# Performance work log

Measured on AMD Instinct MI355X. Metric: run time of the kernel, lower is better.

Reference implementation:

```python
import jax, jax.numpy as jnp
import numpy as np

U = 50  # lstm units

def lstm_seq(x, Wx, Wh, b):
    # x: [B,S,D] -> h: [B,S,U], Keras LSTMCell gate order i,f,g,o
    B = x.shape[0]
    xz = jnp.einsum('bsd,dk->bsk', x, Wx) + b  # [B,S,4U]
    def step(carry, zt):
        h, c = carry
        z = zt + h @ Wh
        i, f, g, o = jnp.split(z, 4, axis=-1)
        c = jax.nn.sigmoid(f) * c + jax.nn.sigmoid(i) * jnp.tanh(g)
        h = jax.nn.sigmoid(o) * jnp.tanh(c)
        return (h, c), h
    init = (jnp.zeros((B, U), x.dtype), jnp.zeros((B, U), x.dtype))
    _, hs = jax.lax.scan(step, init, jnp.swapaxes(xz, 0, 1))
    return jnp.swapaxes(hs, 0, 1)

def bilstm(x, fWx, fWh, fb, bWx, bWh, bb):
    # Keras RNN(go_backwards=True) does NOT re-reverse outputs; concat as-is.
    fw = lstm_seq(x, fWx, fWh, fb)
    bw = lstm_seq(x[:, ::-1, :], bWx, bWh, bb)
    return jnp.concatenate([fw, bw], axis=-1)

def local_inference(x1e, m1, x2e, m2):
    # Literal translation: inputs are batch-first [B,S,D]; the TF code transposes
    # to [S,B,D] and batch-matmuls over the leading (seq) axis, so attention is
    # over the batch index at each timestep. A[s,i,j] = x1e[i,s]. x2e[j,s]
    A = jnp.einsum('isd,jsd->sij', x1e, x2e)
    m1t = m1.T  # [S,B]
    m2t = m2.T
    w2 = jnp.exp(A - jnp.max(A, axis=2, keepdims=True)) * m2t[:, None, :]
    alpha = w2 / (jnp.sum(w2, axis=-1, keepdims=True) + 1e-8)
    x1_dual = jnp.einsum('sij,jsd->isd', alpha, x2e)  # [B,S,D]
    A1 = A - jnp.max(A, axis=1, keepdims=True)
    w1 = jnp.exp(jnp.swapaxes(A1, 1, 2)) * m1t[:, None, :]
    beta = w1 / (jnp.sum(w1, axis=-1, keepdims=True) + 1e-8)
    x2_dual = jnp.einsum('sji,isd->jsd', beta, x1e)  # [B,S,D]
    return x1_dual, x2_dual

def esim_forward(x1, x2, emb, b1f_Wx, b1f_Wh, b1f_b, b1b_Wx, b1b_Wh, b1b_b,
                 dense_W, dense_b, b2f_Wx, b2f_Wh, b2f_b, b2b_Wx, b2b_Wh, b2b_b,
                 dense1_W, dense1_b, out_W, out_b):
    m1 = (x1 != 0).astype(jnp.float32)
    m2 = (x2 != 0).astype(jnp.float32)
    e1 = emb[x1] * m1[..., None]
    e2 = emb[x2] * m2[..., None]
    enc1 = bilstm(e1, b1f_Wx, b1f_Wh, b1f_b, b1b_Wx, b1b_Wh, b1b_b) * m1[..., None]
    enc2 = bilstm(e2, b1f_Wx, b1f_Wh, b1f_b, b1b_Wx, b1b_Wh, b1b_b) * m2[..., None]
    d1, d2 = local_inference(enc1, m1, enc2, m2)
    match1 = jnp.concatenate([enc1, d1, enc1 * d1, enc1 - d1], axis=2)
    match2 = jnp.concatenate([enc2, d2, enc2 * d2, enc2 - d2], axis=2)
    map1 = jax.nn.relu(match1 @ dense_W + dense_b)
    map2 = jax.nn.relu(match2 @ dense_W + dense_b)
    cmp1 = bilstm(map1, b2f_Wx, b2f_Wh, b2f_b, b2b_Wx, b2b_Wh, b2b_b)
    cmp2 = bilstm(map2, b2f_Wx, b2f_Wh, b2f_b, b2b_Wx, b2b_Wh, b2b_b)
    c1m = cmp1 * m1[..., None]
    c2m = cmp2 * m2[..., None]
    p1_sum = jnp.sum(c1m, axis=1) / jnp.sum(m1, axis=1)[:, None]
    p1_max = jnp.max(c1m, axis=1)
    p2_sum = jnp.sum(c2m, axis=1) / jnp.sum(m2, axis=1)[:, None]
    p2_max = jnp.max(c2m, axis=1)
    logit = jnp.concatenate([p1_sum, p1_max, p2_sum, p2_max], axis=1)
    logit = jnp.tanh(logit @ dense1_W + dense1_b)
    logit = logit @ out_W + out_b
    return jax.nn.softmax(logit, axis=-1)

def setup_inputs() -> dict:
    key = jax.random.key(0)
    ks = jax.random.split(key, 24)
    B, S, V, E = 128, 512, 20000, 50
    def w(k, shape, s=0.05):
        return jax.random.normal(k, shape, dtype=jnp.float32) * s
    return {
        'x1': jax.random.randint(ks[0], (B, S), 0, V, dtype=jnp.int32),
        'x2': jax.random.randint(ks[1], (B, S), 0, V, dtype=jnp.int32),
        'emb': jax.random.uniform(ks[2], (V, E), jnp.float32, -0.05, 0.05),
        'b1f_Wx': w(ks[3], (E, 4 * U)), 'b1f_Wh': w(ks[4], (U, 4 * U)), 'b1f_b': w(ks[5], (4 * U,)),
        'b1b_Wx': w(ks[6], (E, 4 * U)), 'b1b_Wh': w(ks[7], (U, 4 * U)), 'b1b_b': w(ks[8], (4 * U,)),
        'dense_W': w(ks[9], (400, 100), 0.02), 'dense_b': jnp.zeros((100,), jnp.float32),
        'b2f_Wx': w(ks[10], (100, 4 * U)), 'b2f_Wh': w(ks[11], (U, 4 * U)), 'b2f_b': w(ks[12], (4 * U,)),
        'b2b_Wx': w(ks[13], (100, 4 * U)), 'b2b_Wh': w(ks[14], (U, 4 * U)), 'b2b_b': w(ks[15], (4 * U,)),
        'dense1_W': w(ks[16], (400, 100), 0.02), 'dense1_b': jnp.zeros((100,), jnp.float32),
        'out_W': w(ks[17], (100, 2), 0.02), 'out_b': jnp.zeros((2,), jnp.float32),
    }

def reference(x1, x2, emb, b1f_Wx, b1f_Wh, b1f_b, b1b_Wx, b1b_Wh, b1b_b,
              dense_W, dense_b, b2f_Wx, b2f_Wh, b2f_b, b2b_Wx, b2b_Wh, b2b_b,
              dense1_W, dense1_b, out_W, out_b):
    return esim_forward(x1, x2, emb, b1f_Wx, b1f_Wh, b1f_b, b1b_Wx, b1b_Wh, b1b_b,
                        dense_W, dense_b, b2f_Wx, b2f_Wh, b2f_b, b2b_Wx, b2b_Wh, b2b_b,
                        dense1_W, dense1_b, out_W, out_b)
```

## Files before the change

### kernel.cpp

```cpp
#include <hip/hip_runtime.h>

#define TOKN 65536
#define SQ 512
#define BB 128
#define DD 100
#define APAD 132

typedef unsigned short bf16t;
typedef __attribute__((ext_vector_type(8))) short bf16x8;
typedef __attribute__((ext_vector_type(4))) float floatx4;
typedef __attribute__((ext_vector_type(2))) _Float16 half2t;

__device__ __forceinline__ float bf2f(bf16t v) {
  unsigned u = ((unsigned)v) << 16;
  return __uint_as_float(u);
}
__device__ __forceinline__ bf16t f2bf(float x) {
  unsigned u = __float_as_uint(x);
  unsigned r = u + 0x7FFFu + ((u >> 16) & 1u);
  return (bf16t)(r >> 16);
}
__device__ __forceinline__ float2 ldpair(const float* p) { return *(const float2*)p; }
__device__ __forceinline__ float2 ldpair(const bf16t* p) {
  unsigned u = *(const unsigned*)p;
  float2 r;
  r.x = __uint_as_float(u << 16);
  r.y = __uint_as_float(u & 0xFFFF0000u);
  return r;
}
__device__ __forceinline__ half2t u2h2(unsigned u) {
  union { unsigned u; half2t h; } x; x.u = u; return x.h;
}

__device__ __forceinline__ float sigm(float x) { return 1.f / (1.f + __expf(-x)); }
__device__ __forceinline__ float tanhx(float x) { return 1.f - 2.f / (1.f + __expf(2.f * x)); }

#if __has_builtin(__builtin_amdgcn_fdot2)
#define DOT2(hu, wu, acc) acc = __builtin_amdgcn_fdot2(u2h2(hu), u2h2(wu), acc, false);
#else
#define DOT2(hu, wu, acc) { half2t hh = u2h2(hu), ww = u2h2(wu); \
  acc = fmaf((float)hh[0], (float)ww[0], acc); \
  acc = fmaf((float)hh[1], (float)ww[1], acc); }
#endif

__global__ __launch_bounds__(256) void embed_kernel(
    const int* __restrict__ x1, const int* __restrict__ x2,
    const float* __restrict__ emb,
    bf16t* __restrict__ e1, bf16t* __restrict__ e2,
    float* __restrict__ m1, float* __restrict__ m2) {
  const int which = blockIdx.y;
  const int* __restrict__ x = which ? x2 : x1;
  bf16t* __restrict__ e = which ? e2 : e1;
  float* __restrict__ m = which ? m2 : m1;
  int idx = blockIdx.x * 256 + threadIdx.x;
  int t = idx >> 6, d = idx & 63;
  int tok = x[t];
  float mk = (tok != 0) ? 1.f : 0.f;
  float v = (d < 50) ? emb[tok * 50 + d] * mk : 0.f;
  e[idx] = f2bf(v);
  if (d == 0) m[t] = mk;
}

__global__ __launch_bounds__(256) void padzero_kernel(
    unsigned* __restrict__ p1, unsigned* __restrict__ p2) {
  int idx = blockIdx.x * 256 + threadIdx.x;
  if (idx >= TOKN * 14) return;
  int t = idx / 14, d = idx - t * 14;
  p1[(size_t)t * 64 + 50 + d] = 0u;
  p2[(size_t)t * 64 + 50 + d] = 0u;
}

__global__ __launch_bounds__(256) void wprep_kernel(
    const float* __restrict__ w1f, const float* __restrict__ w1b,
    const float* __restrict__ w2f, const float* __restrict__ w2b,
    const float* __restrict__ dW,
    const float* __restrict__ h1f, const float* __restrict__ h1b,
    const float* __restrict__ h2f, const float* __restrict__ h2b,
    bf16t* __restrict__ w1T, bf16t* __restrict__ w2T, bf16t* __restrict__ wdT,
    unsigned* __restrict__ whP) {
  int idx = blockIdx.x * 256 + threadIdx.x;
  int sec = blockIdx.y;
  if (sec == 0) {
    if (idx >= 2 * 208 * 64) return;
    int d = idx / (208 * 64), r = idx % (208 * 64);
    int n = r >> 6, k = r & 63;
    const float* W = d ? w1b : w1f;
    float v = (n < 200 && k < 50) ? W[k * 200 + n] : 0.f;
    w1T[idx] = f2bf(v);
  } else if (sec == 1) {
    if (idx >= 2 * 208 * 128) return;
    int d = idx / (208 * 128), r = idx % (208 * 128);
    int n = r >> 7, k = r & 127;
    const float* W = d ? w2b : w2f;
    float v = (n < 200 && k < 100) ? W[k * 200 + n] : 0.f;
    w2T[idx] = f2bf(v);
  } else if (sec == 2) {
    if (idx >= 128 * 384) return;
    int n = idx / 384, kv = idx % 384;
    int reg = kv >> 7, kk = kv & 127;
    float v = 0.f;
    if (n < 100 && kk < 100) {
      if (reg == 0) v = dW[kk * 100 + n] + dW[(300 + kk) * 100 + n];
      else if (reg == 1) v = dW[(100 + kk) * 100 + n] - dW[(300 + kk) * 100 + n];
      else v = dW[(200 + kk) * 100 + n];
    }
    wdT[idx] = f2bf(v);
  } else {
    if (idx >= 4 * 25 * 200) return;
    int sd = idx / 5000, r = idx % 5000;
    int k2 = r / 200, colx = r % 200;
    const float* W = (sd == 0) ? h1f : (sd == 1) ? h1b : (sd == 2) ? h2f : h2b;
    float v0 = W[(2 * k2) * 200 + colx];
    float v1 = W[(2 * k2 + 1) * 200 + colx];
    union { _Float16 h[2]; unsigned u; } p;
    p.h[0] = (_Float16)v0;
    p.h[1] = (_Float16)v1;
    whP[idx] = p.u;
  }
}

template <int KP>
__global__ __launch_bounds__(256) void xz_mfma(
    const bf16t* __restrict__ A1, const bf16t* __restrict__ A2,
    const bf16t* __restrict__ WT,
    const float* __restrict__ bf_, const float* __restrict__ bb_,
    bf16t* __restrict__ out) {
  const int combo = blockIdx.y;
  const bf16t* __restrict__ A = (combo < 2) ? A1 : A2;
  const bf16t* __restrict__ W = WT + (size_t)(combo & 1) * 208 * KP;
  const float* __restrict__ bias = (combo & 1) ? bb_ : bf_;
  bf16t* __restrict__ O = out + (size_t)combo * TOKN * 200;
  const int tid = threadIdx.x;
  const int wave = tid >> 6, lane = tid & 63;
  const int m0 = blockIdx.x * 64 + wave * 16;
  const int l15 = lane & 15, quad = lane >> 4;
  floatx4 acc[13];
#pragma unroll
  for (int nt = 0; nt < 13; ++nt) acc[nt] = (floatx4){0.f, 0.f, 0.f, 0.f};
  const bf16t* __restrict__ arow = A + (size_t)(m0 + l15) * KP + quad * 8;
  const bf16t* __restrict__ wb = W + (size_t)l15 * KP + quad * 8;
#pragma unroll
  for (int ks = 0; ks < KP / 32; ++ks) {
    bf16x8 a = *(const bf16x8*)(arow + ks * 32);
#pragma unroll
    for (int nt = 0; nt < 13; ++nt) {
      bf16x8 b = *(const bf16x8*)(wb + (size_t)nt * 16 * KP + ks * 32);
      acc[nt] = __builtin_amdgcn_mfma_f32_16x16x32_bf16(a, b, acc[nt], 0, 0, 0);
    }
  }
  const int crow = m0 + quad * 4;
  const int bidx = crow >> 9;
  const int trow = crow & 511;
#pragma unroll
  for (int nt = 0; nt < 13; ++nt) {
    int n = nt * 16 + l15;
    if (n < 200) {
      float bn = bias[n];
      union { bf16t h[4]; uint2 u2; } pk;
#pragma unroll
      for (int r = 0; r < 4; ++r) pk.h[r] = f2bf(acc[nt][r] + bn);
      *(uint2*)&O[((size_t)bidx * 200 + n) * SQ + trow] = pk.u2;
    }
  }
}

__global__ __launch_bounds__(256) void dense_mfma(
    const bf16t* __restrict__ enc1, const bf16t* __restrict__ enc2,
    const bf16t* __restrict__ d1b, const bf16t* __restrict__ d2b,
    const bf16t* __restrict__ wdT, const float* __restrict__ bias,
    bf16t* __restrict__ map1, bf16t* __restrict__ map2) {
  const int inp = blockIdx.y;
  const bf16t* __restrict__ E = inp ? enc2 : enc1;
  const bf16t* __restrict__ Db = inp ? d2b : d1b;
  bf16t* __restrict__ O = inp ? map2 : map1;
  const int tid = threadIdx.x;
  const int wave = tid >> 6, lane = tid & 63;
  const int m0 = blockIdx.x * 64 + wave * 16;
  const int l15 = lane & 15, quad = lane >> 4;
  floatx4 acc[8];
#pragma unroll
  for (int nt = 0; nt < 8; ++nt) acc[nt] = (floatx4){0.f, 0.f, 0.f, 0.f};
  const bf16t* __restrict__ erow = E + (size_t)(m0 + l15) * 128 + quad * 8;
  const bf16t* __restrict__ drow = Db + (size_t)(m0 + l15) * 128 + quad * 8;
  const bf16t* __restrict__ wb = wdT + (size_t)l15 * 384 + quad * 8;
#pragma unroll
  for (int ks = 0; ks < 4; ++ks) {
    bf16x8 ae = *(const bf16x8*)(erow + ks * 32);
    bf16x8 ad = *(const bf16x8*)(drow + ks * 32);
    bf16x8 aed;
#pragma unroll
    for (int q = 0; q < 8; ++q) {
      float pe = bf2f((bf16t)ae[q]);
      float pd = bf2f((bf16t)ad[q]);
      aed[q] = (short)f2bf(pe * pd);
    }
#pragma unroll
    for (int nt = 0; nt < 8; ++nt) {
      const bf16t* wn = wb + (size_t)nt * 16 * 384 + ks * 32;
      bf16x8 b0 = *(const bf16x8*)(wn);
      acc[nt] = __builtin_amdgcn_mfma_f32_16x16x32_bf16(ae, b0, acc[nt], 0, 0, 0);
      bf16x8 b1 = *(const bf16x8*)(wn + 128);
      acc[nt] = __builtin_amdgcn_mfma_f32_16x16x32_bf16(ad, b1, acc[nt], 0, 0, 0);
      bf16x8 b2 = *(const bf16x8*)(wn + 256);
      acc[nt] = __builtin_amdgcn_mfma_f32_16x16x32_bf16(aed, b2, acc[nt], 0, 0, 0);
    }
  }
  const int crow = m0 + quad * 4;
#pragma unroll
  for (int nt = 0; nt < 8; ++nt) {
    int n = nt * 16 + l15;
    float bn = (n < 100) ? bias[n] : 0.f;
#pragma unroll
    for (int r = 0; r < 4; ++r) {
      float v = (n < 100) ? fmaxf(acc[nt][r] + bn, 0.f) : 0.f;
      O[(size_t)(crow + r) * 128 + n] = f2bf(v);
    }
  }
}

__global__ __launch_bounds__(64)
__attribute__((amdgpu_waves_per_eu(1, 2)))
void lstm_scan(
    const bf16t* __restrict__ xzT,
    const unsigned* __restrict__ whPL,
    bf16t* __restrict__ out1, bf16t* __restrict__ out2,
    const float* __restrict__ m1, const float* __restrict__ m2,
    int hasMask) {
  const int blk = blockIdx.x;
  const int scan = blk >> 7;
  const int b = blk & 127;
  const int inp = scan >> 1;
  const int dir = scan & 1;
  const int u = threadIdx.x;
  const bool act_l = (u < 50);
  const int uc = act_l ? u : 0;
  const bf16t* __restrict__ xbase = xzT + ((size_t)scan * 128 + b) * 200 * SQ;
  const bf16t* __restrict__ xi = xbase + (size_t)uc * SQ;
  const bf16t* __restrict__ xf = xbase + (size_t)(50 + uc) * SQ;
  const bf16t* __restrict__ xg = xbase + (size_t)(100 + uc) * SQ;
  const bf16t* __restrict__ xo = xbase + (size_t)(150 + uc) * SQ;
  bf16t* __restrict__ outp = (inp ? out2 : out1) + (size_t)b * SQ * 128 + dir * 50;
  const float* __restrict__ mk = (inp ? m2 : m1) + b * SQ;
  __shared__ __align__(16) unsigned hbuf[2][32];

  const unsigned* __restrict__ wsrc = whPL + dir * 5000;
  unsigned wgt[4][25];
#pragma unroll
  for (int gg = 0; gg < 4; ++gg)
#pragma unroll
    for (int k2 = 0; k2 < 25; ++k2)
      wgt[gg][k2] = wsrc[k2 * 200 + gg * 50 + uc];
#pragma unroll
  for (int gg = 0; gg < 4; ++gg)
#pragma unroll
    for (int k2 = 0; k2 < 25; ++k2)
      asm volatile("" : "+v"(wgt[gg][k2]));

  ((unsigned*)hbuf)[u] = 0;
  float c = 0.f;
  const float4* mk4 = (const float4*)mk;

  uint4 zc0, zc1, zc2, zc3, zn0, zn1, zn2, zn3;
  {
    int r0 = dir ? (SQ - 8) : 0;
    int r1 = dir ? (SQ - 16) : 8;
    zc0 = *(const uint4*)(xi + r0); zn0 = *(const uint4*)(xi + r1);
    zc1 = *(const uint4*)(xf + r0); zn1 = *(const uint4*)(xf + r1);
    zc2 = *(const uint4*)(xg + r0); zn2 = *(const uint4*)(xg + r1);
    zc3 = *(const uint4*)(xo + r0); zn3 = *(const uint4*)(xo + r1);
  }

  for (int g8 = 0; g8 < SQ / 8; ++g8) {
    float zst[4][8];
    {
      uint4 cur[4] = {zc0, zc1, zc2, zc3};
#pragma unroll
      for (int gg = 0; gg < 4; ++gg) {
        unsigned dw[4] = {cur[gg].x, cur[gg].y, cur[gg].z, cur[gg].w};
#pragma unroll
        for (int p = 0; p < 4; ++p) {
          float lo = __uint_as_float(dw[p] << 16);
          float hi = __uint_as_float(dw[p] & 0xFFFF0000u);
          if (dir) { zst[gg][7 - 2 * p] = lo; zst[gg][6 - 2 * p] = hi; }
          else     { zst[gg][2 * p] = lo;     zst[gg][2 * p + 1] = hi; }
        }
      }
    }
    uint4 zf0 = zn0, zf1 = zn1, zf2 = zn2, zf3 = zn3;
    {
      int gnext = (g8 + 2 < SQ / 8) ? (g8 + 2) : (SQ / 8 - 1);
      int rn = dir ? (SQ - 8 - 8 * gnext) : (8 * gnext);
      zn0 = *(const uint4*)(xi + rn);
      zn1 = *(const uint4*)(xf + rn);
      zn2 = *(const uint4*)(xg + rn);
      zn3 = *(const uint4*)(xo + rn);
    }
    float mva[8];
    if (hasMask) {
      float4 ma = mk4[2 * g8], mb = mk4[2 * g8 + 1];
      mva[0] = ma.x; mva[1] = ma.y; mva[2] = ma.z; mva[3] = ma.w;
      mva[4] = mb.x; mva[5] = mb.y; mva[6] = mb.z; mva[7] = mb.w;
    }
    bf16t hs8[8];
#pragma unroll
    for (int j = 0; j < 8; ++j) {
      const int par = j & 1;
      const uint4* hp = (const uint4*)&hbuf[par][0];
      uint4 q0 = hp[0], q1 = hp[1], q2 = hp[2], q3 = hp[3], q4 = hp[4], q5 = hp[5];
      unsigned qL = hbuf[par][24];
      unsigned hd[25] = {q0.x, q0.y, q0.z, q0.w, q1.x, q1.y, q1.z, q1.w,
                         q2.x, q2.y, q2.z, q2.w, q3.x, q3.y, q3.z, q3.w,
                         q4.x, q4.y, q4.z, q4.w, q5.x, q5.y, q5.z, q5.w, qL};
      float res[4];
#pragma unroll
      for (int gg = 0; gg < 4; ++gg) {
        float a0 = zst[gg][j], a1 = 0.f;
#pragma unroll
        for (int k2 = 0; k2 < 24; k2 += 2) {
          DOT2(hd[k2], wgt[gg][k2], a0)
          DOT2(hd[k2 + 1], wgt[gg][k2 + 1], a1)
        }
        DOT2(hd[24], wgt[gg][24], a0)
        res[gg] = a0 + a1;
      }
      float ai = sigm(res[0]);
      float af = sigm(res[1]);
      float ag = tanhx(res[2]);
      float ao = sigm(res[3]);
      c = af * c + ai * ag;
      float hn = ao * tanhx(c);
      if (act_l) {
        ((_Float16*)&hbuf[par ^ 1][0])[u] = (_Float16)hn;
        float mv = hasMask ? mva[j] : 1.f;
        hs8[j] = f2bf(hn * mv);
      }
    }
    if (act_l) {
      int t0 = 8 * g8;
#pragma unroll
      for (int j = 0; j < 8; ++j)
        outp[(size_t)(t0 + j) * 128 + u] = hs8[j];
    }
    zc0 = zf0; zc1 = zf1; zc2 = zf2; zc3 = zf3;
  }
}

__global__ __launch_bounds__(256) void attn_kernel(
    const bf16t* __restrict__ enc1, const bf16t* __restrict__ enc2,
    const float* __restrict__ m1, const float* __restrict__ m2,
    bf16t* __restrict__ d1b, bf16t* __restrict__ d2b) {
  const int s = blockIdx.x;
  const int tid = threadIdx.x;
  __shared__ __align__(16) float E1[BB][DD];
  __shared__ __align__(16) float E2[BB + 1][DD];
  __shared__ __align__(16) float Ah[64][APAD];
  __shared__ float mk1[BB], mk2[BB];
  __shared__ float rden[64];

  for (int idx = tid; idx < BB * 50; idx += 256) {
    int i = idx / 50, dp = idx - i * 50;
    float2 v1 = ldpair(enc1 + ((size_t)i * SQ + s) * 128 + 2 * dp);
    E1[i][2 * dp] = v1.x;
    E1[i][2 * dp + 1] = v1.y;
    float2 v2 = ldpair(enc2 + ((size_t)i * SQ + s) * 128 + 2 * dp);
    E2[i][2 * dp] = v2.x;
    E2[i][2 * dp + 1] = v2.y;
  }
  if (tid < BB) {
    mk1[tid] = m1[tid * SQ + s];
    mk2[tid] = m2[tid * SQ + s];
  }
  __syncthreads();

  const int ti = tid >> 4, tjj = tid & 15;
  const int xj = tid & 127;
  const int xd0 = (tid >> 7) * 50;
  float N[50];
#pragma unroll
  for (int q = 0; q < 50; ++q) N[q] = 0.f;
  float Dacc = 0.f, M = -1e30f;

  for (int half = 0; half < 2; ++half) {
    const int r0 = half * 64;
    float acc[4][8];
#pragma unroll
    for (int ii = 0; ii < 4; ++ii)
#pragma unroll
      for (int jj = 0; jj < 8; ++jj) acc[ii][jj] = 0.f;
    for (int k = 0; k < DD; k += 4) {
      float4 a4[4], b4[8];
#pragma unroll
      for (int ii = 0; ii < 4; ++ii)
        a4[ii] = *(const float4*)&E1[r0 + 4 * ti + ii][k];
#pragma unroll
      for (int jj = 0; jj < 8; ++jj)
        b4[jj] = *(const float4*)&E2[tjj + 16 * jj][k];
#pragma unroll
      for (int ii = 0; ii < 4; ++ii)
#pragma unroll
        for (int jj = 0; jj < 8; ++jj)
          acc[ii][jj] += a4[ii].x * b4[jj].x + a4[ii].y * b4[jj].y +
                         a4[ii].z * b4[jj].z + a4[ii].w * b4[jj].w;
    }
#pragma unroll
    for (int ii = 0; ii < 4; ++ii)
#pragma unroll
      for (int jj = 0; jj < 8; ++jj)
        Ah[4 * ti + ii][tjj + 16 * jj] = acc[ii][jj];
    __syncthreads();

    {
      float lm = M;
      for (int i = 0; i < 64; ++i) lm = fmaxf(lm, Ah[i][xj]);
      float scale = __expf(M - lm);
      Dacc *= scale;
#pragma unroll
      for (int q = 0; q < 50; ++q) N[q] *= scale;
      for (int i = 0; i < 64; ++i) {
        float p = __expf(Ah[i][xj] - lm) * mk1[r0 + i];
        Dacc += p;
        const float2* e1p = (const float2*)&E1[r0 + i][xd0];
#pragma unroll
        for (int q = 0; q < 25; ++q) {
          float2 ev = e1p[q];
          N[2 * q] += p * ev.x;
          N[2 * q + 1] += p * ev.y;
        }
      }
      M = lm;
    }
    __syncthreads();

    {
      int row = tid >> 2, seg = tid & 3;
      float mx = -1e30f;
      for (int q = 0; q < 32; ++q) mx = fmaxf(mx, Ah[row][seg + 4 * q]);
      mx = fmaxf(mx, __shfl_xor(mx, 1));
      mx = fmaxf(mx, __shfl_xor(mx, 2));
      float sm = 0.f;
      for (int q = 0; q < 32; ++q) {
        int jc = seg + 4 * q;
        float p = __expf(Ah[row][jc] - mx) * mk2[jc];
        Ah[row][jc] = p;
        sm += p;
      }
      sm += __shfl_xor(sm, 1);
      sm += __shfl_xor(sm, 2);
      if (seg == 0) rden[row] = sm + 1e-8f;
    }
    __syncthreads();

    {
      const int ri = tid >> 4, cg = tid & 15;
      float o[4][8];
#pragma unroll
      for (int ii = 0; ii < 4; ++ii)
#pragma unroll
        for (int jj = 0; jj < 8; ++jj) o[ii][jj] = 0.f;
      for (int jb = 0; jb < BB; jb += 4) {
        float4 pv[4];
#pragma unroll
        for (int ii = 0; ii < 4; ++ii)
          pv[ii] = *(const float4*)&Ah[4 * ri + ii][jb];
#pragma unroll
        for (int q = 0; q < 4; ++q) {
          float4 e0 = *(const float4*)&E2[jb + q][8 * cg];
          float4 e1v = *(const float4*)&E2[jb + q][8 * cg + 4];
          float ev[8] = {e0.x, e0.y, e0.z, e0.w, e1v.x, e1v.y, e1v.z, e1v.w};
#pragma unroll
          for (int ii = 0; ii < 4; ++ii) {
            float p = (q == 0) ? pv[ii].x : (q == 1) ? pv[ii].y
                     : (q == 2) ? pv[ii].z : pv[ii].w;
#pragma unroll
            for (int jj = 0; jj < 8; ++jj) o[ii][jj] = fmaf(p, ev[jj], o[ii][jj]);
          }
        }
      }
#pragma unroll
      for (int ii = 0; ii < 4; ++ii) {
        int i = r0 + 4 * ri + ii;
        float inv = 1.f / rden[4 * ri + ii];
        union { bf16t h[8]; uint4 u4; } pk;
#pragma unroll
        for (int jj = 0; jj < 8; ++jj) {
          int d = 8 * cg + jj;
          pk.h[jj] = (d < DD) ? f2bf(o[ii][jj] * inv) : (bf16t)0;
        }
        *(uint4*)&d1b[((size_t)i * SQ + s) * 128 + 8 * cg] = pk.u4;
      }
    }
    __syncthreads();
  }
  float invD = 1.f / (Dacc + 1e-8f);
#pragma unroll
  for (int q = 0; q < 50; ++q)
    d2b[((size_t)xj * SQ + s) * 128 + xd0 + q] = f2bf(N[q] * invD);
  if (xd0 == 50) {
#pragma unroll
    for (int q = 0; q < 28; ++q)
      d2b[((size_t)xj * SQ + s) * 128 + 100 + q] = 0;
  }
}

__global__ __launch_bounds__(128) void pool_kernel(
    const bf16t* __restrict__ cmp1, const bf16t* __restrict__ cmp2,
    const float* __restrict__ m1, const float* __restrict__ m2,
    float* __restrict__ pooled) {
  int b = blockIdx.x & 127, inp = blockIdx.x >> 7;
  const bf16t* C = (inp ? cmp2 : cmp1) + (size_t)b * SQ * 128;
  const float* M = (inp ? m2 : m1) + b * SQ;
  int f = threadIdx.x;
  float ms = 0.f;
  for (int s = f; s < SQ; s += 128) ms += M[s];
  __shared__ float red[128];
  red[f] = ms;
  __syncthreads();
  for (int o = 64; o > 0; o >>= 1) {
    if (f < o) red[f] += red[f + o];
    __syncthreads();
  }
  float msum = red[0];
  if (f < 100) {
    float sm = 0.f, mx = -1e30f;
    for (int s = 0; s < SQ; ++s) {
      float v = bf2f(C[(size_t)s * 128 + f]) * M[s];
      sm += v;
      mx = fmaxf(mx, v);
    }
    pooled[b * 400 + inp * 200 + f] = sm / msum;
    pooled[b * 400 + inp * 200 + 100 + f] = mx;
  }
}

__global__ __launch_bounds__(128) void final_kernel(
    const float* __restrict__ pooled, const float* __restrict__ W1,
    const float* __restrict__ b1, const float* __restrict__ W2,
    const float* __restrict__ b2, float* __restrict__ out) {
  int b = blockIdx.x;
  int j = threadIdx.x;
  __shared__ float pr[400];
  __shared__ float h[100];
  for (int idx = j; idx < 400; idx += 128) pr[idx] = pooled[b * 400 + idx];
  __syncthreads();
  if (j < 100) {
    float a = b1[j];
    for (int k = 0; k < 400; ++k) a += pr[k] * W1[k * 100 + j];
    h[j] = tanhx(a);
  }
  __syncthreads();
  if (j == 0) {
    float l0 = b2[0], l1 = b2[1];
    for (int k = 0; k < 100; ++k) {
      l0 += h[k] * W2[k * 2];
      l1 += h[k] * W2[k * 2 + 1];
    }
    float mx = fmaxf(l0, l1);
    float e0 = __expf(l0 - mx), e1 = __expf(l1 - mx);
    float inv = 1.f / (e0 + e1);
    out[b * 2] = e0 * inv;
    out[b * 2 + 1] = e1 * inv;
  }
}

extern "C" void kernel_launch(void* const* d_in, const int* in_sizes, int n_in,
                              void* d_out, int out_size, void* d_ws, size_t ws_size,
                              hipStream_t stream) {
  const int* x1 = (const int*)d_in[0];
  const int* x2 = (const int*)d_in[1];
  const float* emb = (const float*)d_in[2];
  const float* b1f_Wx = (const float*)d_in[3];
  const float* b1f_Wh = (const float*)d_in[4];
  const float* b1f_b = (const float*)d_in[5];
  const float* b1b_Wx = (const float*)d_in[6];
  const float* b1b_Wh = (const float*)d_in[7];
  const float* b1b_b = (const float*)d_in[8];
  const float* dense_W = (const float*)d_in[9];
  const float* dense_b = (const float*)d_in[10];
  const float* b2f_Wx = (const float*)d_in[11];
  const float* b2f_Wh = (const float*)d_in[12];
  const float* b2f_b = (const float*)d_in[13];
  const float* b2b_Wx = (const float*)d_in[14];
  const float* b2b_Wh = (const float*)d_in[15];
  const float* b2b_b = (const float*)d_in[16];
  const float* dense1_W = (const float*)d_in[17];
  const float* dense1_b = (const float*)d_in[18];
  const float* out_W = (const float*)d_in[19];
  const float* out_b = (const float*)d_in[20];
  float* out = (float*)d_out;

  char* base = (char*)d_ws;
  bf16t* xz = (bf16t*)base;
  bf16t* d1b = (bf16t*)base;
  bf16t* d2b = d1b + (size_t)TOKN * 128;
  char* r1 = base + (size_t)4 * TOKN * 200 * 2;
  bf16t* enc1 = (bf16t*)r1;
  bf16t* enc2 = enc1 + (size_t)TOKN * 128;
  bf16t* e1b = (bf16t*)r1;
  bf16t* e2b = e1b + (size_t)TOKN * 64;
  char* r2 = r1 + (size_t)2 * TOKN * 128 * 2;
  bf16t* map1 = (bf16t*)r2;
  bf16t* map2 = map1 + (size_t)TOKN * 128;
  char* r3 = r2 + (size_t)2 * TOKN * 128 * 2;
  float* m1 = (float*)r3;
  float* m2 = m1 + TOKN;
  float* pooled = m2 + TOKN;
  bf16t* w1T = (bf16t*)(r3 + ((size_t)2 * TOKN + 128 * 400) * 4);
  bf16t* w2T = w1T + 2 * 208 * 64;
  bf16t* wdT = w2T + 2 * 208 * 128;
  unsigned* whP = (unsigned*)(wdT + 128 * 384);
  bf16t* cmp1 = enc1;
  bf16t* cmp2 = enc2;
  (void)in_sizes; (void)n_in; (void)out_size; (void)ws_size;

  embed_kernel<<<dim3(TOKN * 64 / 256, 2), 256, 0, stream>>>(
      x1, x2, emb, e1b, e2b, m1, m2);
  wprep_kernel<<<dim3(208, 4), 256, 0, stream>>>(
      b1f_Wx, b1b_Wx, b2f_Wx, b2b_Wx, dense_W,
      b1f_Wh, b1b_Wh, b2f_Wh, b2b_Wh, w1T, w2T, wdT, whP);
  xz_mfma<64><<<dim3(TOKN / 64, 4), 256, 0, stream>>>(
      e1b, e2b, w1T, b1f_b, b1b_b, xz);
  padzero_kernel<<<(TOKN * 14 + 255) / 256, 256, 0, stream>>>(
      (unsigned*)enc1, (unsigned*)enc2);
  lstm_scan<<<512, 64, 0, stream>>>(xz, whP, enc1, enc2, m1, m2, 1);
  attn_kernel<<<SQ, 256, 0, stream>>>(enc1, enc2, m1, m2, d1b, d2b);
  dense_mfma<<<dim3(TOKN / 64, 2), 256, 0, stream>>>(
      enc1, enc2, d1b, d2b, wdT, dense_b, map1, map2);
  xz_mfma<128><<<dim3(TOKN / 64, 4), 256, 0, stream>>>(
      map1, map2, w2T, b2f_b, b2b_b, xz);
  lstm_scan<<<512, 64, 0, stream>>>(xz, whP + 2 * 5000, cmp1, cmp2, m1, m2, 0);
  pool_kernel<<<256, 128, 0, stream>>>(cmp1, cmp2, m1, m2, pooled);
  final_kernel<<<128, 128, 0, stream>>>(pooled, dense1_W, dense1_b, out_W, out_b, out);
}
```

Baseline: 1.052 ms.

## Use fp16 shared tiles and packed dot2/half2 math in attention kernel

Converts the attention kernel's shared-memory copies of enc1/enc2 from fp32 to fp16, with padded rows, and loads only the current half of enc1 per iteration. It computes the score matmul with fdot2 and the two weighted-sum accumulations with packed half2 FMAs, and vectorizes the d2 stores. This is meant to cut LDS footprint and bandwidth and to raise ALU throughput. The half2 accumulators (N2, o2) lose precision and range compared with fp32 accumulation, which could hurt accuracy.

```diff
diff --git a/kernel.cpp b/kernel.cpp
--- a/kernel.cpp
+++ b/kernel.cpp
@@ -30,6 +30,12 @@
 }
 __device__ __forceinline__ half2t u2h2(unsigned u) {
   union { unsigned u; half2t h; } x; x.u = u; return x.h;
+}
+__device__ __forceinline__ unsigned h2u(half2t h) {
+  union { half2t h; unsigned u; } x; x.h = h; return x.u;
+}
+__device__ __forceinline__ half2t f2h2(float a) {
+  half2t h; h[0] = (_Float16)a; h[1] = (_Float16)a; return h;
 }
 
 __device__ __forceinline__ float sigm(float x) { return 1.f / (1.f + __expf(-x)); }
@@ -351,56 +357,77 @@
     bf16t* __restrict__ d1b, bf16t* __restrict__ d2b) {
   const int s = blockIdx.x;
   const int tid = threadIdx.x;
-  __shared__ __align__(16) float E1[BB][DD];
-  __shared__ __align__(16) float E2[BB + 1][DD];
+  __shared__ __align__(16) _Float16 E1h[64][104];
+  __shared__ __align__(16) _Float16 E2h[BB][104];
   __shared__ __align__(16) float Ah[64][APAD];
   __shared__ float mk1[BB], mk2[BB];
   __shared__ float rden[64];
 
   for (int idx = tid; idx < BB * 50; idx += 256) {
     int i = idx / 50, dp = idx - i * 50;
-    float2 v1 = ldpair(enc1 + ((size_t)i * SQ + s) * 128 + 2 * dp);
-    E1[i][2 * dp] = v1.x;
-    E1[i][2 * dp + 1] = v1.y;
-    float2 v2 = ldpair(enc2 + ((size_t)i * SQ + s) * 128 + 2 * dp);
-    E2[i][2 * dp] = v2.x;
-    E2[i][2 * dp + 1] = v2.y;
+    unsigned uu = *(const unsigned*)&enc2[((size_t)i * SQ + s) * 128 + 2 * dp];
+    half2t h;
+    h[0] = (_Float16)__uint_as_float(uu << 16);
+    h[1] = (_Float16)__uint_as_float(uu & 0xFFFF0000u);
+    *(unsigned*)&E2h[i][2 * dp] = h2u(h);
+  }
+  {
+    int i = tid >> 1, cpad = tid & 1;
+    *(unsigned*)&E2h[i][100 + 2 * cpad] = 0u;
   }
   if (tid < BB) {
     mk1[tid] = m1[tid * SQ + s];
     mk2[tid] = m2[tid * SQ + s];
   }
-  __syncthreads();
 
   const int ti = tid >> 4, tjj = tid & 15;
   const int xj = tid & 127;
   const int xd0 = (tid >> 7) * 50;
-  float N[50];
-#pragma unroll
-  for (int q = 0; q < 50; ++q) N[q] = 0.f;
+  half2t N2[25];
+#pragma unroll
+  for (int q = 0; q < 25; ++q) N2[q] = (half2t){(_Float16)0.f, (_Float16)0.f};
   float Dacc = 0.f, M = -1e30f;
 
   for (int half = 0; half < 2; ++half) {
     const int r0 = half * 64;
+    __syncthreads();
+    for (int idx = tid; idx < 64 * 50; idx += 256) {
+      int i = idx / 50, dp = idx - i * 50;
+      unsigned uu = *(const unsigned*)&enc1[((size_t)(r0 + i) * SQ + s) * 128 + 2 * dp];
+      half2t h;
+      h[0] = (_Float16)__uint_as_float(uu << 16);
+      h[1] = (_Float16)__uint_as_float(uu & 0xFFFF0000u);
+      *(unsigned*)&E1h[i][2 * dp] = h2u(h);
+    }
+    if (tid < 128) {
+      int i = tid >> 1, cpad = tid & 1;
+      *(unsigned*)&E1h[i][100 + 2 * cpad] = 0u;
+    }
+    __syncthreads();
+
     float acc[4][8];
 #pragma unroll
     for (int ii = 0; ii < 4; ++ii)
 #pragma unroll
       for (int jj = 0; jj < 8; ++jj) acc[ii][jj] = 0.f;
-    for (int k = 0; k < DD; k += 4) {
-      float4 a4[4], b4[8];
+#pragma unroll
+    for (int kc = 0; kc < 13; ++kc) {
+      uint4 a4[4], b4[8];
 #pragma unroll
       for (int ii = 0; ii < 4; ++ii)
-        a4[ii] = *(const float4*)&E1[r0 + 4 * ti + ii][k];
+        a4[ii] = *(const uint4*)&E1h[4 * ti + ii][8 * kc];
 #pragma unroll
       for (int jj = 0; jj < 8; ++jj)
-        b4[jj] = *(const float4*)&E2[tjj + 16 * jj][k];
+        b4[jj] = *(const uint4*)&E2h[tjj + 16 * jj][8 * kc];
 #pragma unroll
       for (int ii = 0; ii < 4; ++ii)
 #pragma unroll
-        for (int jj = 0; jj < 8; ++jj)
-          acc[ii][jj] += a4[ii].x * b4[jj].x + a4[ii].y * b4[jj].y +
-                         a4[ii].z * b4[jj].z + a4[ii].w * b4[jj].w;
+        for (int jj = 0; jj < 8; ++jj) {
+          DOT2(a4[ii].x, b4[jj].x, acc[ii][jj])
+          DOT2(a4[ii].y, b4[jj].y, acc[ii][jj])
+          DOT2(a4[ii].z, b4[jj].z, acc[ii][jj])
+          DOT2(a4[ii].w, b4[jj].w, acc[ii][jj])
+        }
     }
 #pragma unroll
     for (int ii = 0; ii < 4; ++ii)
@@ -414,18 +441,16 @@
       for (int i = 0; i < 64; ++i) lm = fmaxf(lm, Ah[i][xj]);
       float scale = __expf(M - lm);
       Dacc *= scale;
-#pragma unroll
-      for (int q = 0; q < 50; ++q) N[q] *= scale;
+      half2t sc2 = f2h2(scale);
+#pragma unroll
+      for (int q = 0; q < 25; ++q) N2[q] *= sc2;
       for (int i = 0; i < 64; ++i) {
         float p = __expf(Ah[i][xj] - lm) * mk1[r0 + i];
         Dacc += p;
-        const float2* e1p = (const float2*)&E1[r0 + i][xd0];
-#pragma unroll
-        for (int q = 0; q < 25; ++q) {
-          float2 ev = e1p[q];
-          N[2 * q] += p * ev.x;
-          N[2 * q + 1] += p * ev.y;
-        }
+        half2t p2 = f2h2(p);
+        const unsigned* e1p = (const unsigned*)&E1h[i][xd0];
+#pragma unroll
+        for (int q = 0; q < 25; ++q) N2[q] += u2h2(e1p[q]) * p2;
       }
       M = lm;
     }
@@ -452,27 +477,31 @@
 
     {
       const int ri = tid >> 4, cg = tid & 15;
-      float o[4][8];
+      half2t o2[4][4];
 #pragma unroll
       for (int ii = 0; ii < 4; ++ii)
 #pragma unroll
-        for (int jj = 0; jj < 8; ++jj) o[ii][jj] = 0.f;
+        for (int k = 0; k < 4; ++k) o2[ii][k] = (half2t){(_Float16)0.f, (_Float16)0.f};
+      const int cgc = (cg < 13) ? cg : 0;
       for (int jb = 0; jb < BB; jb += 4) {
         float4 pv[4];
 #pragma unroll
         for (int ii = 0; ii < 4; ++ii)
           pv[ii] = *(const float4*)&Ah[4 * ri + ii][jb];
+        uint4 e4[4];
+#pragma unroll
+        for (int q = 0; q < 4; ++q)
+          e4[q] = *(const uint4*)&E2h[jb + q][8 * cgc];
 #pragma unroll
         for (int q = 0; q < 4; ++q) {
-          float4 e0 = *(const float4*)&E2[jb + q][8 * cg];
-          float4 e1v = *(const float4*)&E2[jb + q][8 * cg + 4];
-          float ev[8] = {e0.x, e0.y, e0.z, e0.w, e1v.x, e1v.y, e1v.z, e1v.w};
+          unsigned ee[4] = {e4[q].x, e4[q].y, e4[q].z, e4[q].w};
 #pragma unroll
           for (int ii = 0; ii < 4; ++ii) {
             float p = (q == 0) ? pv[ii].x : (q == 1) ? pv[ii].y
                      : (q == 2) ? pv[ii].z : pv[ii].w;
-#pragma unroll
-            for (int jj = 0; jj < 8; ++jj) o[ii][jj] = fmaf(p, ev[jj], o[ii][jj]);
+            half2t p2 = f2h2(p);
+#pragma unroll
+            for (int k = 0; k < 4; ++k) o2[ii][k] += u2h2(ee[k]) * p2;
           }
         }
       }
@@ -481,24 +510,35 @@
         int i = r0 + 4 * ri + ii;
         float inv = 1.f / rden[4 * ri + ii];
         union { bf16t h[8]; uint4 u4; } pk;
-#pragma unroll
-        for (int jj = 0; jj < 8; ++jj) {
-          int d = 8 * cg + jj;
-          pk.h[jj] = (d < DD) ? f2bf(o[ii][jj] * inv) : (bf16t)0;
+        if (cg < 13) {
+#pragma unroll
+          for (int jj = 0; jj < 8; ++jj) {
+            int d = 8 * cg + jj;
+            float v = (float)o2[ii][jj >> 1][jj & 1] * inv;
+            pk.h[jj] = (d < DD) ? f2bf(v) : (bf16t)0;
+          }
+        } else {
+#pragma unroll
+          for (int jj = 0; jj < 8; ++jj) pk.h[jj] = 0;
         }
         *(uint4*)&d1b[((size_t)i * SQ + s) * 128 + 8 * cg] = pk.u4;
       }
     }
-    __syncthreads();
   }
   float invD = 1.f / (Dacc + 1e-8f);
 #pragma unroll
-  for (int q = 0; q < 50; ++q)
-    d2b[((size_t)xj * SQ + s) * 128 + xd0 + q] = f2bf(N[q] * invD);
+  for (int q = 0; q < 25; ++q) {
+    float f0 = (float)N2[q][0] * invD;
+    float f1 = (float)N2[q][1] * invD;
+    union { bf16t h[2]; unsigned u; } pk;
+    pk.h[0] = f2bf(f0);
+    pk.h[1] = f2bf(f1);
+    *(unsigned*)&d2b[((size_t)xj * SQ + s) * 128 + xd0 + 2 * q] = pk.u;
+  }
   if (xd0 == 50) {
 #pragma unroll
-    for (int q = 0; q < 28; ++q)
-      d2b[((size_t)xj * SQ + s) * 128 + 100 + q] = 0;
+    for (int q = 0; q < 14; ++q)
+      *(unsigned*)&d2b[((size_t)xj * SQ + s) * 128 + 100 + 2 * q] = 0u;
   }
 }
 
```

New measurement: 1.040 ms. About the same (-1.1%).
